# Kernel optimization log

Hardware: AMD Instinct MI355X
Metric: run time of the kernel (lower is better)

The kernel has to match this reference:

```python
import jax, jax.numpy as jnp
import numpy as np

B = 256
D, H, W = 15, 64, 128    # depth, latitude, longitude of input grid
d, h, w = 5, 16, 32      # grid after AveragePooling3D(3,4,4)
L_DEPTH = (d + 2) * h * w      # 3584
L_LON   = d * h * (w + 2)      # 2720
L_LAT   = d * (h + 2) * w      # 2880


def _local1d(xp, wt, bias):
    # Unshared-weight LocallyConnected1D(filters=1, kernel=3) + relu.
    # xp: (B, L+2) padded sequence; wt: (L, 3); bias: (L,)
    L = wt.shape[0]
    y = (wt[:, 0] * xp[:, 0:L]
         + wt[:, 1] * xp[:, 1:L + 1]
         + wt[:, 2] * xp[:, 2:L + 2]
         + bias)
    return jax.nn.relu(y)


def setup_inputs() -> dict:
    key = jax.random.key(0)
    ks = jax.random.split(key, 7)
    s = 0.1
    return {
        "x": jax.random.normal(ks[0], (B, D, H, W, 1), jnp.float32),
        "w_depth": jax.random.normal(ks[1], (L_DEPTH, 3), jnp.float32) * s,
        "b_depth": jax.random.normal(ks[2], (L_DEPTH,), jnp.float32) * s,
        "w_lon": jax.random.normal(ks[3], (L_LON, 3), jnp.float32) * s,
        "b_lon": jax.random.normal(ks[4], (L_LON,), jnp.float32) * s,
        "w_lat": jax.random.normal(ks[5], (L_LAT, 3), jnp.float32) * s,
        "b_lat": jax.random.normal(ks[6], (L_LAT,), jnp.float32) * s,
    }


def reference(x, w_depth, b_depth, w_lon, b_lon, w_lat, b_lat):
    Bn = x.shape[0]
    # AveragePooling3D(3,4,4): dims divide evenly -> reshape + mean
    xs = x.reshape(Bn, d, 3, h, 4, w, 4, 1).mean(axis=(2, 4, 6))  # (B,d,h,w,1)

    # ---- depth axis: pad depth, permute (3,2,1,4), flatten, local conv ----
    t = jnp.pad(xs, ((0, 0), (1, 1), (0, 0), (0, 0), (0, 0)))     # (B,d+2,h,w,1)
    t = jnp.transpose(t, (0, 3, 2, 1, 4))                         # (B,w,h,d+2,1)
    t = t.reshape(Bn, L_DEPTH)
    t = jnp.pad(t, ((0, 0), (1, 1)))                              # ZeroPadding1D(1)
    t = _local1d(t, w_depth, b_depth)
    t = t.reshape(Bn, w, h, d + 2, 1)
    t = jnp.transpose(t, (0, 3, 2, 1, 4))                         # (B,d+2,h,w,1)
    t = t[:, 1:-1]                                                # crop depth -> (B,d,h,w,1)

    # ---- longitude axis: pad last spatial dim, identity permute ----
    u = jnp.pad(t, ((0, 0), (0, 0), (0, 0), (1, 1), (0, 0)))      # (B,d,h,w+2,1)
    u = u.reshape(Bn, L_LON)
    u = jnp.pad(u, ((0, 0), (1, 1)))
    u = _local1d(u, w_lon, b_lon)
    u = u.reshape(Bn, d, h, w + 2, 1)
    u = u[:, :, :, 1:-1]                                          # (B,d,h,w,1)

    # ---- latitude axis: pad lat, permute (1,3,2,4) ----
    v = jnp.pad(u, ((0, 0), (0, 0), (1, 1), (0, 0), (0, 0)))      # (B,d,h+2,w,1)
    v = jnp.transpose(v, (0, 1, 3, 2, 4))                         # (B,d,w,h+2,1)
    v = v.reshape(Bn, L_LAT)
    v = jnp.pad(v, ((0, 0), (1, 1)))
    v = _local1d(v, w_lat, b_lat)
    v = v.reshape(Bn, d, w, h + 2, 1)
    v = jnp.transpose(v, (0, 1, 3, 2, 4))                         # (B,d,h+2,w,1)
    v = v[:, :, 1:-1]                                             # (B,d,h,w,1)

    # UpSampling3D(3,4,4): nearest-neighbor repeat
    out = jnp.broadcast_to(
        v[:, :, None, :, None, :, None, :],
        (Bn, d, 3, h, 4, w, 4, 1)
    ).reshape(Bn, D, H, W, 1)
    return out
```

## Files before the change

kernel.cpp:

```cpp
#include <hip/hip_runtime.h>


#define NELEM (15 * 64 * 128)
#define NCELL 2560
#define LD    3584
#define LLON  2720
#define LLAT  2880

__global__ __launch_bounds__(256) void k_down(const float* __restrict__ x,
                                              float* __restrict__ ds)
{
    const int b  = blockIdx.y;
    const int c  = blockIdx.x * 256 + threadIdx.x;
    const int iw = c & 31;
    const int ih = (c >> 5) & 15;
    const int id = c >> 9;

    const float* p = x + (size_t)b * NELEM + ((id * 3) * 64 + ih * 4) * 128 + iw * 4;
    float s = 0.f;
    #pragma unroll
    for (int dd = 0; dd < 3; ++dd) {
        #pragma unroll
        for (int hh = 0; hh < 4; ++hh) {
            const float4 v = *reinterpret_cast<const float4*>(p + (dd * 64 + hh) * 128);
            s += (v.x + v.y) + (v.z + v.w);
        }
    }
    ds[(size_t)b * NCELL + c] = s * (1.f / 48.f);
}

__device__ __forceinline__ float tf_depth(const float* __restrict__ dsb, int f)
{
    const int k  = f % 7;
    const int q  = f / 7;
    const int ih = q & 15;
    const int iw = q >> 4;
    return (k >= 1 && k <= 5) ? dsb[((k - 1) * 16 + ih) * 32 + iw] : 0.f;
}

__global__ __launch_bounds__(256) void k_depth(const float* __restrict__ ds,
                                               const float* __restrict__ w,
                                               const float* __restrict__ bias,
                                               float* __restrict__ t1)
{
    const int b = blockIdx.y;
    const int l = blockIdx.x * 256 + threadIdx.x;
    const float* dsb = ds + (size_t)b * NCELL;

    const float x0 = (l > 0)      ? tf_depth(dsb, l - 1) : 0.f;
    const float x1 =                tf_depth(dsb, l);
    const float x2 = (l < LD - 1) ? tf_depth(dsb, l + 1) : 0.f;
    const float y  = w[l * 3] * x0 + w[l * 3 + 1] * x1 + w[l * 3 + 2] * x2 + bias[l];
    t1[(size_t)b * LD + l] = fmaxf(y, 0.f);
}

__device__ __forceinline__ float uf_lon(const float* __restrict__ t1b, int f)
{
    const int kw  = f % 34;
    const int q   = f / 34;
    const int ih  = q & 15;
    const int dep = q >> 4;
    return (kw >= 1 && kw <= 32) ? t1b[((kw - 1) * 16 + ih) * 7 + dep + 1] : 0.f;
}

__global__ __launch_bounds__(256) void k_lon(const float* __restrict__ t1,
                                             const float* __restrict__ w,
                                             const float* __restrict__ bias,
                                             float* __restrict__ u1)
{
    const int b = blockIdx.y;
    const int m = blockIdx.x * 256 + threadIdx.x;
    if (m >= LLON) return;
    const float* t1b = t1 + (size_t)b * LD;

    const float x0 = (m > 0)        ? uf_lon(t1b, m - 1) : 0.f;
    const float x1 =                  uf_lon(t1b, m);
    const float x2 = (m < LLON - 1) ? uf_lon(t1b, m + 1) : 0.f;
    const float y  = w[m * 3] * x0 + w[m * 3 + 1] * x1 + w[m * 3 + 2] * x2 + bias[m];
    u1[(size_t)b * LLON + m] = fmaxf(y, 0.f);
}

__device__ __forceinline__ float vf_lat(const float* __restrict__ u1b, int f)
{
    const int kh  = f % 18;
    const int q   = f / 18;
    const int iw  = q & 31;
    const int dep = q >> 5;
    return (kh >= 1 && kh <= 16) ? u1b[(dep * 16 + kh - 1) * 34 + iw + 1] : 0.f;
}

__global__ __launch_bounds__(256) void k_lat_up(const float* __restrict__ u1,
                                                const float* __restrict__ w,
                                                const float* __restrict__ bias,
                                                float* __restrict__ out)
{
    const int b   = blockIdx.y;
    const int o   = blockIdx.x * 256 + threadIdx.x;
    const int iww = o & 31;
    const int Hin = (o >> 5) & 63;
    const int Din = o >> 11;
    const int dep = Din / 3;
    const int ihh = Hin >> 2;
    const int n   = (dep * 32 + iww) * 18 + ihh + 1;

    const float* u1b = u1 + (size_t)b * LLON;
    const float x0 = vf_lat(u1b, n - 1);
    const float x1 = vf_lat(u1b, n);
    const float x2 = vf_lat(u1b, n + 1);
    const float y  = fmaxf(w[n * 3] * x0 + w[n * 3 + 1] * x1 + w[n * 3 + 2] * x2 + bias[n], 0.f);

    *reinterpret_cast<float4*>(out + (size_t)b * NELEM + (size_t)o * 4) =
        make_float4(y, y, y, y);
}

extern "C" void kernel_launch(void* const* d_in, const int* in_sizes, int n_in,
                              void* d_out, int out_size, void* d_ws, size_t ws_size,
                              hipStream_t stream) {
    const float* x       = (const float*)d_in[0];
    const float* w_depth = (const float*)d_in[1];
    const float* b_depth = (const float*)d_in[2];
    const float* w_lon   = (const float*)d_in[3];
    const float* b_lon   = (const float*)d_in[4];
    const float* w_lat   = (const float*)d_in[5];
    const float* b_lat   = (const float*)d_in[6];
    float* out = (float*)d_out;

    const int Bn = in_sizes[0] / NELEM;

    float* ds = (float*)d_ws;
    float* t1 = ds + (size_t)Bn * NCELL;
    float* u1 = t1 + (size_t)Bn * LD;

    k_down  <<<dim3(NCELL / 256, Bn), dim3(256), 0, stream>>>(x, ds);
    k_depth <<<dim3(LD / 256, Bn),    dim3(256), 0, stream>>>(ds, w_depth, b_depth, t1);
    k_lon   <<<dim3((LLON + 255) / 256, Bn), dim3(256), 0, stream>>>(t1, w_lon, b_lon, u1);
    k_lat_up<<<dim3(NELEM / 4 / 256, Bn), dim3(256), 0, stream>>>(u1, w_lat, b_lat, out);
}
```

Baseline: 247.1 us.

## Fuse depth conv into lon kernel and compute lat once per cell

The depth local-conv kernel is removed and its values are recomputed inline inside the longitude kernel, dropping one launch and the t1 intermediate buffer. The lat+upsample kernel now computes each coarse cell once and writes its 12 float4 replicas, instead of one thread per output float4 recomputing the lat conv. This cuts redundant conv arithmetic and gathers in the output stage. The cost is recomputing each depth value roughly three times in the middle kernel and a less contiguous store pattern per thread.

```diff
diff --git a/kernel.cpp b/kernel.cpp
--- a/kernel.cpp
+++ b/kernel.cpp
@@ -5,7 +5,6 @@
 #define NCELL 2560
 #define LD    3584
 #define LLON  2720
-#define LLAT  2880
 
 __global__ __launch_bounds__(256) void k_down(const float* __restrict__ x,
                                               float* __restrict__ ds)
@@ -38,45 +37,44 @@
     return (k >= 1 && k <= 5) ? dsb[((k - 1) * 16 + ih) * 32 + iw] : 0.f;
 }
 
-__global__ __launch_bounds__(256) void k_depth(const float* __restrict__ ds,
-                                               const float* __restrict__ w,
-                                               const float* __restrict__ bias,
-                                               float* __restrict__ t1)
+__device__ __forceinline__ float t1_val(const float* __restrict__ dsb,
+                                        const float* __restrict__ wd,
+                                        const float* __restrict__ bd, int l)
 {
-    const int b = blockIdx.y;
-    const int l = blockIdx.x * 256 + threadIdx.x;
-    const float* dsb = ds + (size_t)b * NCELL;
-
     const float x0 = (l > 0)      ? tf_depth(dsb, l - 1) : 0.f;
     const float x1 =                tf_depth(dsb, l);
     const float x2 = (l < LD - 1) ? tf_depth(dsb, l + 1) : 0.f;
-    const float y  = w[l * 3] * x0 + w[l * 3 + 1] * x1 + w[l * 3 + 2] * x2 + bias[l];
-    t1[(size_t)b * LD + l] = fmaxf(y, 0.f);
+    return fmaxf(wd[l * 3] * x0 + wd[l * 3 + 1] * x1 + wd[l * 3 + 2] * x2 + bd[l], 0.f);
 }
 
-__device__ __forceinline__ float uf_lon(const float* __restrict__ t1b, int f)
+__device__ __forceinline__ float uf_lon(const float* __restrict__ dsb,
+                                        const float* __restrict__ wd,
+                                        const float* __restrict__ bd, int f)
 {
     const int kw  = f % 34;
     const int q   = f / 34;
     const int ih  = q & 15;
     const int dep = q >> 4;
-    return (kw >= 1 && kw <= 32) ? t1b[((kw - 1) * 16 + ih) * 7 + dep + 1] : 0.f;
+    if (kw < 1 || kw > 32) return 0.f;
+    return t1_val(dsb, wd, bd, ((kw - 1) * 16 + ih) * 7 + dep + 1);
 }
 
-__global__ __launch_bounds__(256) void k_lon(const float* __restrict__ t1,
-                                             const float* __restrict__ w,
-                                             const float* __restrict__ bias,
+__global__ __launch_bounds__(256) void k_mid(const float* __restrict__ ds,
+                                             const float* __restrict__ wd,
+                                             const float* __restrict__ bd,
+                                             const float* __restrict__ wl,
+                                             const float* __restrict__ bl,
                                              float* __restrict__ u1)
 {
     const int b = blockIdx.y;
     const int m = blockIdx.x * 256 + threadIdx.x;
     if (m >= LLON) return;
-    const float* t1b = t1 + (size_t)b * LD;
+    const float* dsb = ds + (size_t)b * NCELL;
 
-    const float x0 = (m > 0)        ? uf_lon(t1b, m - 1) : 0.f;
-    const float x1 =                  uf_lon(t1b, m);
-    const float x2 = (m < LLON - 1) ? uf_lon(t1b, m + 1) : 0.f;
-    const float y  = w[m * 3] * x0 + w[m * 3 + 1] * x1 + w[m * 3 + 2] * x2 + bias[m];
+    const float x0 = (m > 0)        ? uf_lon(dsb, wd, bd, m - 1) : 0.f;
+    const float x1 =                  uf_lon(dsb, wd, bd, m);
+    const float x2 = (m < LLON - 1) ? uf_lon(dsb, wd, bd, m + 1) : 0.f;
+    const float y  = wl[m * 3] * x0 + wl[m * 3 + 1] * x1 + wl[m * 3 + 2] * x2 + bl[m];
     u1[(size_t)b * LLON + m] = fmaxf(y, 0.f);
 }
 
@@ -89,18 +87,16 @@
     return (kh >= 1 && kh <= 16) ? u1b[(dep * 16 + kh - 1) * 34 + iw + 1] : 0.f;
 }
 
-__global__ __launch_bounds__(256) void k_lat_up(const float* __restrict__ u1,
-                                                const float* __restrict__ w,
-                                                const float* __restrict__ bias,
-                                                float* __restrict__ out)
+__global__ __launch_bounds__(256) void k_vup(const float* __restrict__ u1,
+                                             const float* __restrict__ w,
+                                             const float* __restrict__ bias,
+                                             float* __restrict__ out)
 {
     const int b   = blockIdx.y;
-    const int o   = blockIdx.x * 256 + threadIdx.x;
-    const int iww = o & 31;
-    const int Hin = (o >> 5) & 63;
-    const int Din = o >> 11;
-    const int dep = Din / 3;
-    const int ihh = Hin >> 2;
+    const int c   = blockIdx.x * 256 + threadIdx.x;
+    const int iww = c & 31;
+    const int ihh = (c >> 5) & 15;
+    const int dep = c >> 9;
     const int n   = (dep * 32 + iww) * 18 + ihh + 1;
 
     const float* u1b = u1 + (size_t)b * LLON;
@@ -108,9 +104,16 @@
     const float x1 = vf_lat(u1b, n);
     const float x2 = vf_lat(u1b, n + 1);
     const float y  = fmaxf(w[n * 3] * x0 + w[n * 3 + 1] * x1 + w[n * 3 + 2] * x2 + bias[n], 0.f);
+    const float4 y4 = make_float4(y, y, y, y);
 
-    *reinterpret_cast<float4*>(out + (size_t)b * NELEM + (size_t)o * 4) =
-        make_float4(y, y, y, y);
+    float4* ob = reinterpret_cast<float4*>(out + (size_t)b * NELEM);
+    #pragma unroll
+    for (int dd = 0; dd < 3; ++dd) {
+        #pragma unroll
+        for (int hh = 0; hh < 4; ++hh) {
+            ob[((dep * 3 + dd) * 64 + ihh * 4 + hh) * 32 + iww] = y4;
+        }
+    }
 }
 
 extern "C" void kernel_launch(void* const* d_in, const int* in_sizes, int n_in,
@@ -128,11 +131,10 @@
     const int Bn = in_sizes[0] / NELEM;
 
     float* ds = (float*)d_ws;
-    float* t1 = ds + (size_t)Bn * NCELL;
-    float* u1 = t1 + (size_t)Bn * LD;
+    float* u1 = ds + (size_t)Bn * NCELL;
 
-    k_down  <<<dim3(NCELL / 256, Bn), dim3(256), 0, stream>>>(x, ds);
-    k_depth <<<dim3(LD / 256, Bn),    dim3(256), 0, stream>>>(ds, w_depth, b_depth, t1);
-    k_lon   <<<dim3((LLON + 255) / 256, Bn), dim3(256), 0, stream>>>(t1, w_lon, b_lon, u1);
-    k_lat_up<<<dim3(NELEM / 4 / 256, Bn), dim3(256), 0, stream>>>(u1, w_lat, b_lat, out);
+    k_down<<<dim3(NCELL / 256, Bn), dim3(256), 0, stream>>>(x, ds);
+    k_mid <<<dim3((LLON + 255) / 256, Bn), dim3(256), 0, stream>>>(ds, w_depth, b_depth,
+                                                                   w_lon, b_lon, u1);
+    k_vup <<<dim3(NCELL / 256, Bn), dim3(256), 0, stream>>>(u1, w_lat, b_lat, out);
 }
```

Result: faster. 242.0 us (-2.1%).
